# Optimization experiments

Measured on AMD Instinct MI355X. Metric: run time of the kernel, lower is better.

The kernel has to match this reference:

```python
import jax, jax.numpy as jnp
import numpy as np

E = 23  # unique experts
K = 3   # activated experts per token


def setup_inputs() -> dict:
    key = jax.random.key(0)
    ks = jax.random.split(key, 8)
    B, S, D, H = 4, 1024, 1024, 768
    sd = 1.0 / np.sqrt(D)
    sh = 1.0 / np.sqrt(H)
    return {
        "x": jax.random.normal(ks[0], (B, S, D), jnp.float32),
        "gate_W": jax.random.normal(ks[1], (D, E), jnp.float32) * sd,
        "gate_b": jnp.zeros((E,), jnp.float32),
        "route_bias": jnp.zeros((E,), jnp.float32),  # registered buffer 'bias'
        "W1": jax.random.normal(ks[2], (E, D, H), jnp.float32) * sd,
        "b1": jnp.zeros((E, H), jnp.float32),
        "W2": jax.random.normal(ks[3], (E, H, D), jnp.float32) * sh,
        "b2": jnp.zeros((E, D), jnp.float32),
        "sW1": jax.random.normal(ks[4], (D, H), jnp.float32) * sd,
        "sb1": jnp.zeros((H,), jnp.float32),
        "sW2": jax.random.normal(ks[5], (H, D), jnp.float32) * sh,
        "sb2": jnp.zeros((D,), jnp.float32),
    }


def _gelu(x):
    return jax.nn.gelu(x, approximate=False)  # torch nn.GELU default = exact erf


def reference(x, gate_W, gate_b, route_bias, W1, b1, W2, b2, sW1, sb1, sW2, sb2):
    o_shape = x.shape
    xt = x.reshape(-1, o_shape[-1])                       # [N, D]
    N = xt.shape[0]
    gate_weights = jax.nn.sigmoid(xt @ gate_W + gate_b)   # [N, E]
    _, top_idx = jax.lax.top_k(gate_weights + route_bias, K)  # [N, K]
    top_w = jnp.take_along_axis(gate_weights, top_idx, axis=-1)
    top_w = top_w / top_w.sum(axis=-1, keepdims=True)     # [N, K]
    onehot = jax.nn.one_hot(top_idx, E, dtype=xt.dtype)   # [N, K, E]
    combine = jnp.einsum('nke,nk->ne', onehot, top_w)     # [N, E] routed weights
    counts = onehot.sum(axis=(0, 1))                      # tokens per expert
    # dense-equivalent grouped expert MLPs (same math as gather/split/concat)
    h = _gelu(jnp.einsum('nd,edh->enh', xt, W1) + b1[:, None, :])   # [E, N, H]
    y = jnp.einsum('enh,ehd->end', h, W2) + b2[:, None, :]          # [E, N, D]
    routed = jnp.einsum('end,ne->nd', y, combine)
    shared = _gelu(xt @ sW1 + sb1) @ sW2 + sb2
    out = shared + routed
    # aux load-balance loss
    gw_norm = gate_weights / gate_weights.sum(axis=-1, keepdims=True)
    P = gw_norm.mean(axis=0)
    Fvec = (E * counts) / (K * N)
    aux_loss = (P * Fvec).sum()
    return out.reshape(o_shape), aux_loss
```

## Files before the change

kernel.cpp:

```cpp
#include <hip/hip_runtime.h>
#include <hip/hip_bf16.h>
#include <stdint.h>

#define N_TOK 4096
#define DDIM  1024
#define HDIM  768
#define NEXP  23
#define TOPK  3
#define MAXTILE 152
#define SLOTS   19456

typedef float floatx4 __attribute__((ext_vector_type(4)));
typedef short short8  __attribute__((ext_vector_type(8)));

__device__ __forceinline__ short f2bf(float f) {
    __hip_bfloat16 h = __float2bfloat16(f);
    return *reinterpret_cast<short*>(&h);
}
__device__ __forceinline__ float bf2f(short s) {
    unsigned u = ((unsigned)(unsigned short)s) << 16;
    return __uint_as_float(u);
}
__device__ __forceinline__ float gelu_erf(float v) {
    return 0.5f * v * (1.0f + erff(v * 0.70710678118654752f));
}
__device__ __forceinline__ void gl_lds16(const short* g, short* l) {
    __builtin_amdgcn_global_load_lds(
        (const __attribute__((address_space(1))) void*)g,
        (__attribute__((address_space(3))) void*)l, 16, 0, 0);
}

__global__ __launch_bounds__(256) void gate_kernel(
    const float* __restrict__ x, const float* __restrict__ gate_W,
    const float* __restrict__ gate_b, const float* __restrict__ route_bias,
    int* __restrict__ top_idx, float* __restrict__ top_w,
    float* __restrict__ psum_part)
{
    const int wave = threadIdx.x >> 6, lane = threadIdx.x & 63;
    const int n = blockIdx.x * 4 + wave;

    __shared__ float gw[64][25];
    float acc[NEXP];
#pragma unroll
    for (int e = 0; e < NEXP; e++) acc[e] = 0.f;

    const float* xr = x + (size_t)n * DDIM;
    for (int c0 = 0; c0 < DDIM; c0 += 64) {
        for (int idx = threadIdx.x; idx < 64 * NEXP; idx += 256)
            gw[idx / NEXP][idx % NEXP] = gate_W[(size_t)c0 * NEXP + idx];
        __syncthreads();
        float xd = xr[c0 + lane];
#pragma unroll
        for (int e = 0; e < NEXP; e++) acc[e] += xd * gw[lane][e];
        __syncthreads();
    }
    for (int off = 32; off > 0; off >>= 1) {
#pragma unroll
        for (int e = 0; e < NEXP; e++) acc[e] += __shfl_xor(acc[e], off, 64);
    }

    float p[NEXP], s = 0.f;
#pragma unroll
    for (int e = 0; e < NEXP; e++) {
        p[e] = 1.f / (1.f + expf(-(acc[e] + gate_b[e])));
        s += p[e];
    }
    const float inv = 1.f / s;

    __shared__ float ps[4][NEXP];
    if (lane == 0) {
#pragma unroll
        for (int e = 0; e < NEXP; e++) ps[wave][e] = p[e] * inv;
        int idx[TOPK]; float w[TOPK]; bool used[NEXP] = {};
        for (int k = 0; k < TOPK; k++) {
            float best = -1e30f; int bi = 0;
            for (int e = 0; e < NEXP; e++) {
                if (!used[e]) {
                    float sc = p[e] + route_bias[e];
                    if (sc > best) { best = sc; bi = e; }
                }
            }
            used[bi] = true; idx[k] = bi; w[k] = p[bi];
        }
        float wsum = w[0] + w[1] + w[2];
        for (int k = 0; k < TOPK; k++) {
            top_idx[n * TOPK + k] = idx[k];
            top_w[n * TOPK + k]   = w[k] / wsum;
        }
    }
    __syncthreads();
    if (threadIdx.x < NEXP) {
        int e = threadIdx.x;
        psum_part[(size_t)blockIdx.x * NEXP + e] =
            ps[0][e] + ps[1][e] + ps[2][e] + ps[3][e];
    }
}

__global__ __launch_bounds__(256) void plan_kernel(
    const int* __restrict__ top_idx, const float* __restrict__ psum_part,
    int* __restrict__ poff, int* __restrict__ cursor, int* __restrict__ tile_e,
    int* __restrict__ Ptot, float* __restrict__ out_aux)
{
    __shared__ int   cnt[NEXP];
    __shared__ float psum[NEXP];
    const int t = threadIdx.x;
    if (t < NEXP) { cnt[t] = 0; psum[t] = 0.f; }
    __syncthreads();

    for (int i = t; i < N_TOK * TOPK; i += 256)
        atomicAdd(&cnt[top_idx[i]], 1);

    float loc[NEXP];
#pragma unroll
    for (int e = 0; e < NEXP; e++) loc[e] = 0.f;
    for (int b = t; b < N_TOK / 4; b += 256) {
        const float* row = psum_part + (size_t)b * NEXP;
#pragma unroll
        for (int e = 0; e < NEXP; e++) loc[e] += row[e];
    }
#pragma unroll
    for (int e = 0; e < NEXP; e++) atomicAdd(&psum[e], loc[e]);
    __syncthreads();

    if (t == 0) {
        int off = 0, nt = 0; float aux = 0.f;
        for (int e = 0; e < NEXP; e++) {
            poff[e] = off; cursor[e] = 0;
            float P = psum[e] / (float)N_TOK;
            float F = (float)NEXP * (float)cnt[e] / ((float)TOPK * (float)N_TOK);
            aux += P * F;
            int tiles = (cnt[e] + 127) >> 7;
            for (int i = 0; i < tiles; i++) tile_e[nt++] = e;
            off += tiles << 7;
        }
        poff[NEXP] = off;
        *Ptot = off;
        for (int i = 0; i < N_TOK / 128; i++) tile_e[nt++] = NEXP;
        while (nt < MAXTILE) tile_e[nt++] = -1;
        *out_aux = aux;
    }
}

__global__ __launch_bounds__(256) void scatter_kernel(
    const int* __restrict__ top_idx, const int* __restrict__ poff,
    int* __restrict__ cursor, int* __restrict__ tok_of_slot,
    int* __restrict__ slot_of_tok)
{
    int n = blockIdx.x * 256 + threadIdx.x;
    for (int k = 0; k < TOPK; k++) {
        int e = top_idx[n * TOPK + k];
        int pos = atomicAdd(&cursor[e], 1);
        int slot = poff[e] + pos;
        tok_of_slot[slot] = n;
        slot_of_tok[n * 4 + k] = slot;
    }
}

__global__ __launch_bounds__(256) void fillshared_kernel(
    const int* __restrict__ Ptot, int* __restrict__ tok_of_slot,
    int* __restrict__ slot_of_tok)
{
    int n = blockIdx.x * 256 + threadIdx.x;
    int P = *Ptot;
    tok_of_slot[P + n] = n;
    slot_of_tok[n * 4 + 3] = P + n;
}

__global__ __launch_bounds__(256) void xcvt_kernel(
    const float* __restrict__ x, short* __restrict__ xb)
{
    size_t i = (size_t)blockIdx.x * 256 + threadIdx.x;
    float4 v = ((const float4*)x)[i];
    short4 o;
    o.x = f2bf(v.x); o.y = f2bf(v.y); o.z = f2bf(v.z); o.w = f2bf(v.w);
    ((short4*)xb)[i] = o;
    if (blockIdx.x == 0) {
        short4 z; z.x = 0; z.y = 0; z.z = 0; z.w = 0;
        ((short4*)(xb + (size_t)N_TOK * DDIM))[threadIdx.x] = z;
    }
}

__global__ __launch_bounds__(256) void tcvt_kernel(
    const float* __restrict__ src, short* __restrict__ dst, int R, int C)
{
    __shared__ short tile[64][66];
    const float* s = src + (size_t)blockIdx.z * R * C;
    short* d = dst + (size_t)blockIdx.z * R * C;
    const int c0 = blockIdx.x * 64, r0 = blockIdx.y * 64;
    const int tc = threadIdx.x & 63, tq = threadIdx.x >> 6;

    for (int i = 0; i < 64; i += 4) {
        int r = i + tq;
        tile[tc][r] = f2bf(s[(size_t)(r0 + r) * C + c0 + tc]);
    }
    __syncthreads();
    for (int j = 0; j < 64; j += 4) {
        int c = j + tq;
        d[(size_t)(c0 + c) * R + r0 + tc] = tile[c][tc];
    }
}

__global__ __launch_bounds__(256) void biascat_kernel(
    const float* __restrict__ b1, const float* __restrict__ sb1,
    const float* __restrict__ b2, const float* __restrict__ sb2,
    float* __restrict__ bias1_all, float* __restrict__ bias2_all)
{
    int i = blockIdx.x * 256 + threadIdx.x;
    if (i < 24 * HDIM) {
        bias1_all[i] = (i < NEXP * HDIM) ? b1[i] : sb1[i - NEXP * HDIM];
    } else {
        int j = i - 24 * HDIM;
        bias2_all[j] = (j < NEXP * DDIM) ? b2[j] : sb2[j - NEXP * DDIM];
    }
}

template <bool FFN1>
__global__ __launch_bounds__(256) void gemm_kernel(
    const short* __restrict__ Abase, const int* __restrict__ tok_of_slot,
    const int* __restrict__ tile_e, const short* __restrict__ Wall,
    const float* __restrict__ bias_all, const short* __restrict__ zrow,
    short* __restrict__ outb)
{
    constexpr int KD = FFN1 ? DDIM : HDIM;
    constexpr int NC = FFN1 ? HDIM : DDIM;

    const int tile = blockIdx.y;
    const int e = tile_e[tile];
    if (e < 0) return;
    const int slot0 = tile * 128;
    const int n0 = blockIdx.x * 128;

    __shared__ short As[128 * 32];
    __shared__ short Bs[128 * 32];

    const int t = threadIdx.x;
    const int w = t >> 6, l = t & 63;
    const int quad = l >> 4, l16 = l & 15;
    const int wr = w >> 1, wc = w & 1;

    const int ra0 = w * 32 + (l >> 2);
    const int ra1 = ra0 + 16;
    const int ko  = (l & 3) << 3;

    const short *ap0, *ap1;
    if constexpr (FFN1) {
        int t0 = tok_of_slot[slot0 + ra0];
        int t1 = tok_of_slot[slot0 + ra1];
        ap0 = (t0 >= 0) ? Abase + (size_t)t0 * KD : zrow;
        ap1 = (t1 >= 0) ? Abase + (size_t)t1 * KD : zrow;
    } else {
        ap0 = Abase + (size_t)(slot0 + ra0) * KD;
        ap1 = Abase + (size_t)(slot0 + ra1) * KD;
    }
    ap0 += ko; ap1 += ko;
    const short* bbase = Wall + (size_t)e * NC * KD + (size_t)n0 * KD;
    const short* bp0 = bbase + (size_t)ra0 * KD + ko;
    const short* bp1 = bbase + (size_t)ra1 * KD + ko;

    short* asd0 = As + (w * 32) * 32;
    short* asd1 = As + (w * 32 + 16) * 32;
    short* bsd0 = Bs + (w * 32) * 32;
    short* bsd1 = Bs + (w * 32 + 16) * 32;

    floatx4 acc[4][4] = {};

    for (int k0 = 0; k0 < KD; k0 += 32) {
        gl_lds16(ap0, asd0); gl_lds16(ap1, asd1);
        gl_lds16(bp0, bsd0); gl_lds16(bp1, bsd1);
        ap0 += 32; ap1 += 32; bp0 += 32; bp1 += 32;
        __syncthreads();

        short8 af[4], bf[4];
#pragma unroll
        for (int i = 0; i < 4; i++)
            af[i] = *(const short8*)&As[(wr * 64 + i * 16 + l16) * 32 + quad * 8];
#pragma unroll
        for (int j = 0; j < 4; j++)
            bf[j] = *(const short8*)&Bs[(wc * 64 + j * 16 + l16) * 32 + quad * 8];
#pragma unroll
        for (int i = 0; i < 4; i++)
#pragma unroll
            for (int j = 0; j < 4; j++)
                acc[i][j] = __builtin_amdgcn_mfma_f32_16x16x32_bf16(af[i], bf[j], acc[i][j], 0, 0, 0);
        __syncthreads();
    }

    const int bias_off = e * NC;
#pragma unroll
    for (int j = 0; j < 4; j++) {
        const int col = n0 + wc * 64 + j * 16 + l16;
        const float bv = bias_all[bias_off + col];
#pragma unroll
        for (int i = 0; i < 4; i++)
#pragma unroll
            for (int r = 0; r < 4; r++) {
                const int row = slot0 + wr * 64 + i * 16 + quad * 4 + r;
                float v = acc[i][j][r] + bv;
                outb[(size_t)row * NC + col] = f2bf(FFN1 ? gelu_erf(v) : v);
            }
    }
}

__global__ __launch_bounds__(256) void combine_kernel(
    const short* __restrict__ ybuf, const int* __restrict__ slot_of_tok,
    const float* __restrict__ top_w, float* __restrict__ out)
{
    const int n = blockIdx.x;
    const int c = threadIdx.x;
    const int s0 = slot_of_tok[n * 4 + 0];
    const int s1 = slot_of_tok[n * 4 + 1];
    const int s2 = slot_of_tok[n * 4 + 2];
    const int ss = slot_of_tok[n * 4 + 3];
    const float w0 = top_w[n * 3 + 0];
    const float w1 = top_w[n * 3 + 1];
    const float w2 = top_w[n * 3 + 2];

    short4 y0 = ((const short4*)(ybuf + (size_t)s0 * DDIM))[c];
    short4 y1 = ((const short4*)(ybuf + (size_t)s1 * DDIM))[c];
    short4 y2 = ((const short4*)(ybuf + (size_t)s2 * DDIM))[c];
    short4 ys = ((const short4*)(ybuf + (size_t)ss * DDIM))[c];

    float4 o;
    o.x = bf2f(ys.x) + w0 * bf2f(y0.x) + w1 * bf2f(y1.x) + w2 * bf2f(y2.x);
    o.y = bf2f(ys.y) + w0 * bf2f(y0.y) + w1 * bf2f(y1.y) + w2 * bf2f(y2.y);
    o.z = bf2f(ys.z) + w0 * bf2f(y0.z) + w1 * bf2f(y1.z) + w2 * bf2f(y2.z);
    o.w = bf2f(ys.w) + w0 * bf2f(y0.w) + w1 * bf2f(y1.w) + w2 * bf2f(y2.w);
    ((float4*)(out + (size_t)n * DDIM))[c] = o;
}

extern "C" void kernel_launch(void* const* d_in, const int* in_sizes, int n_in,
                              void* d_out, int out_size, void* d_ws, size_t ws_size,
                              hipStream_t stream)
{
    const float* x          = (const float*)d_in[0];
    const float* gate_W     = (const float*)d_in[1];
    const float* gate_b     = (const float*)d_in[2];
    const float* route_bias = (const float*)d_in[3];
    const float* W1         = (const float*)d_in[4];
    const float* b1         = (const float*)d_in[5];
    const float* W2         = (const float*)d_in[6];
    const float* b2         = (const float*)d_in[7];
    const float* sW1        = (const float*)d_in[8];
    const float* sb1        = (const float*)d_in[9];
    const float* sW2        = (const float*)d_in[10];
    const float* sb2        = (const float*)d_in[11];
    float* out = (float*)d_out;

    uint8_t* ws = (uint8_t*)d_ws;
    int*   top_idx   = (int*)(ws);
    float* top_w     = (float*)(ws + 49152);
    int*   poff      = (int*)(ws + 98304);
    int*   cursor    = (int*)(ws + 98432);
    int*   Ptot      = (int*)(ws + 98560);
    int*   tile_e    = (int*)(ws + 98688);
    float* psum_part = (float*)(ws + 99328);
    int*   tok_slot  = (int*)(ws + 193536);
    int*   slot_tok  = (int*)(ws + 271360);
    float* bias1_all = (float*)(ws + 336896);
    float* bias2_all = (float*)(ws + 410624);
    short* xb        = (short*)(ws + 512000);
    short* W1T       = (short*)(ws + 8902656);
    short* W2T       = (short*)(ws + 46651392);
    short* hbuf      = (short*)(ws + 84400128);
    short* ybuf      = (short*)(ws + 512000);
    const short* zrow = xb + (size_t)N_TOK * DDIM;

    hipMemsetAsync(tok_slot, 0xFF, SLOTS * sizeof(int), stream);

    xcvt_kernel<<<N_TOK * DDIM / 4 / 256, 256, 0, stream>>>(x, xb);
    tcvt_kernel<<<dim3(HDIM / 64, DDIM / 64, NEXP), 256, 0, stream>>>(W1, W1T, DDIM, HDIM);
    tcvt_kernel<<<dim3(HDIM / 64, DDIM / 64, 1), 256, 0, stream>>>(
        sW1, W1T + (size_t)NEXP * DDIM * HDIM, DDIM, HDIM);
    tcvt_kernel<<<dim3(DDIM / 64, HDIM / 64, NEXP), 256, 0, stream>>>(W2, W2T, HDIM, DDIM);
    tcvt_kernel<<<dim3(DDIM / 64, HDIM / 64, 1), 256, 0, stream>>>(
        sW2, W2T + (size_t)NEXP * HDIM * DDIM, HDIM, DDIM);
    biascat_kernel<<<(24 * HDIM + 24 * DDIM) / 256, 256, 0, stream>>>(
        b1, sb1, b2, sb2, bias1_all, bias2_all);

    gate_kernel<<<N_TOK / 4, 256, 0, stream>>>(x, gate_W, gate_b, route_bias,
                                               top_idx, top_w, psum_part);
    plan_kernel<<<1, 256, 0, stream>>>(top_idx, psum_part, poff, cursor, tile_e,
                                       Ptot, out + (size_t)N_TOK * DDIM);
    scatter_kernel<<<N_TOK / 256, 256, 0, stream>>>(top_idx, poff, cursor,
                                                    tok_slot, slot_tok);
    fillshared_kernel<<<N_TOK / 256, 256, 0, stream>>>(Ptot, tok_slot, slot_tok);

    gemm_kernel<true><<<dim3(HDIM / 128, MAXTILE), 256, 0, stream>>>(
        xb, tok_slot, tile_e, W1T, bias1_all, zrow, hbuf);
    gemm_kernel<false><<<dim3(DDIM / 128, MAXTILE), 256, 0, stream>>>(
        hbuf, tok_slot, tile_e, W2T, bias2_all, zrow, ybuf);
    combine_kernel<<<N_TOK, 256, 0, stream>>>(ybuf, slot_tok, top_w, out);
}
```

Measured before the change: 503.1 us.

## Vectorize weight transpose-convert and merge small prep launches

New measurement: 492.6 us. 1.02x faster.

```diff
diff --git a/kernel.cpp b/kernel.cpp
--- a/kernel.cpp
+++ b/kernel.cpp
@@ -144,7 +144,7 @@
 __global__ __launch_bounds__(256) void scatter_kernel(
     const int* __restrict__ top_idx, const int* __restrict__ poff,
     int* __restrict__ cursor, int* __restrict__ tok_of_slot,
-    int* __restrict__ slot_of_tok)
+    int* __restrict__ slot_of_tok, const int* __restrict__ Ptot)
 {
     int n = blockIdx.x * 256 + threadIdx.x;
     for (int k = 0; k < TOPK; k++) {
@@ -154,63 +154,65 @@
         tok_of_slot[slot] = n;
         slot_of_tok[n * 4 + k] = slot;
     }
-}
-
-__global__ __launch_bounds__(256) void fillshared_kernel(
-    const int* __restrict__ Ptot, int* __restrict__ tok_of_slot,
-    int* __restrict__ slot_of_tok)
-{
-    int n = blockIdx.x * 256 + threadIdx.x;
     int P = *Ptot;
     tok_of_slot[P + n] = n;
     slot_of_tok[n * 4 + 3] = P + n;
 }
 
-__global__ __launch_bounds__(256) void xcvt_kernel(
-    const float* __restrict__ x, short* __restrict__ xb)
-{
-    size_t i = (size_t)blockIdx.x * 256 + threadIdx.x;
-    float4 v = ((const float4*)x)[i];
-    short4 o;
-    o.x = f2bf(v.x); o.y = f2bf(v.y); o.z = f2bf(v.z); o.w = f2bf(v.w);
-    ((short4*)xb)[i] = o;
-    if (blockIdx.x == 0) {
-        short4 z; z.x = 0; z.y = 0; z.z = 0; z.w = 0;
-        ((short4*)(xb + (size_t)N_TOK * DDIM))[threadIdx.x] = z;
-    }
-}
-
-__global__ __launch_bounds__(256) void tcvt_kernel(
-    const float* __restrict__ src, short* __restrict__ dst, int R, int C)
-{
-    __shared__ short tile[64][66];
-    const float* s = src + (size_t)blockIdx.z * R * C;
-    short* d = dst + (size_t)blockIdx.z * R * C;
-    const int c0 = blockIdx.x * 64, r0 = blockIdx.y * 64;
-    const int tc = threadIdx.x & 63, tq = threadIdx.x >> 6;
-
-    for (int i = 0; i < 64; i += 4) {
-        int r = i + tq;
-        tile[tc][r] = f2bf(s[(size_t)(r0 + r) * C + c0 + tc]);
-    }
-    __syncthreads();
-    for (int j = 0; j < 64; j += 4) {
-        int c = j + tq;
-        d[(size_t)(c0 + c) * R + r0 + tc] = tile[c][tc];
-    }
-}
-
-__global__ __launch_bounds__(256) void biascat_kernel(
+__global__ __launch_bounds__(256) void prep_kernel(
+    const float* __restrict__ x, short* __restrict__ xb,
     const float* __restrict__ b1, const float* __restrict__ sb1,
     const float* __restrict__ b2, const float* __restrict__ sb2,
     float* __restrict__ bias1_all, float* __restrict__ bias2_all)
 {
-    int i = blockIdx.x * 256 + threadIdx.x;
-    if (i < 24 * HDIM) {
-        bias1_all[i] = (i < NEXP * HDIM) ? b1[i] : sb1[i - NEXP * HDIM];
+    const int b = blockIdx.x;
+    if (b < N_TOK) {
+        size_t i = (size_t)b * 256 + threadIdx.x;
+        float4 v = ((const float4*)x)[i];
+        short4 o;
+        o.x = f2bf(v.x); o.y = f2bf(v.y); o.z = f2bf(v.z); o.w = f2bf(v.w);
+        ((short4*)xb)[i] = o;
+    } else if (b == N_TOK) {
+        short4 z; z.x = 0; z.y = 0; z.z = 0; z.w = 0;
+        ((short4*)(xb + (size_t)N_TOK * DDIM))[threadIdx.x] = z;
     } else {
-        int j = i - 24 * HDIM;
-        bias2_all[j] = (j < NEXP * DDIM) ? b2[j] : sb2[j - NEXP * DDIM];
+        int i = (b - N_TOK - 1) * 256 + threadIdx.x;
+        if (i < 24 * HDIM) {
+            bias1_all[i] = (i < NEXP * HDIM) ? b1[i] : sb1[i - NEXP * HDIM];
+        } else {
+            int j = i - 24 * HDIM;
+            if (j < 24 * DDIM)
+                bias2_all[j] = (j < NEXP * DDIM) ? b2[j] : sb2[j - NEXP * DDIM];
+        }
+    }
+}
+
+__global__ __launch_bounds__(256) void tcvt_kernel(
+    const float* __restrict__ src, const float* __restrict__ ssrc,
+    short* __restrict__ dst, int R, int C)
+{
+    __shared__ short tile[64][72];
+    const int e = blockIdx.z;
+    const float* s = (e < NEXP) ? src + (size_t)e * R * C : ssrc;
+    short* d = dst + (size_t)e * R * C;
+    const int c0 = blockIdx.x * 64, r0 = blockIdx.y * 64;
+    const int t = threadIdx.x;
+
+    const int rr = t >> 4, cc = (t & 15) << 2;
+#pragma unroll
+    for (int i = 0; i < 64; i += 16) {
+        float4 v = *(const float4*)&s[(size_t)(r0 + i + rr) * C + c0 + cc];
+        tile[cc + 0][i + rr] = f2bf(v.x);
+        tile[cc + 1][i + rr] = f2bf(v.y);
+        tile[cc + 2][i + rr] = f2bf(v.z);
+        tile[cc + 3][i + rr] = f2bf(v.w);
+    }
+    __syncthreads();
+    const int cc2 = t >> 3, rr2 = (t & 7) << 3;
+#pragma unroll
+    for (int j = 0; j < 64; j += 32) {
+        *(short8*)&d[(size_t)(c0 + j + cc2) * R + r0 + rr2] =
+            *(const short8*)&tile[j + cc2][rr2];
     }
 }
 
@@ -367,23 +369,19 @@
 
     hipMemsetAsync(tok_slot, 0xFF, SLOTS * sizeof(int), stream);
 
-    xcvt_kernel<<<N_TOK * DDIM / 4 / 256, 256, 0, stream>>>(x, xb);
-    tcvt_kernel<<<dim3(HDIM / 64, DDIM / 64, NEXP), 256, 0, stream>>>(W1, W1T, DDIM, HDIM);
-    tcvt_kernel<<<dim3(HDIM / 64, DDIM / 64, 1), 256, 0, stream>>>(
-        sW1, W1T + (size_t)NEXP * DDIM * HDIM, DDIM, HDIM);
-    tcvt_kernel<<<dim3(DDIM / 64, HDIM / 64, NEXP), 256, 0, stream>>>(W2, W2T, HDIM, DDIM);
-    tcvt_kernel<<<dim3(DDIM / 64, HDIM / 64, 1), 256, 0, stream>>>(
-        sW2, W2T + (size_t)NEXP * HDIM * DDIM, HDIM, DDIM);
-    biascat_kernel<<<(24 * HDIM + 24 * DDIM) / 256, 256, 0, stream>>>(
-        b1, sb1, b2, sb2, bias1_all, bias2_all);
+    prep_kernel<<<N_TOK + 1 + (24 * (HDIM + DDIM) + 255) / 256, 256, 0, stream>>>(
+        x, xb, b1, sb1, b2, sb2, bias1_all, bias2_all);
+    tcvt_kernel<<<dim3(HDIM / 64, DDIM / 64, 24), 256, 0, stream>>>(
+        W1, sW1, W1T, DDIM, HDIM);
+    tcvt_kernel<<<dim3(DDIM / 64, HDIM / 64, 24), 256, 0, stream>>>(
+        W2, sW2, W2T, HDIM, DDIM);
 
     gate_kernel<<<N_TOK / 4, 256, 0, stream>>>(x, gate_W, gate_b, route_bias,
                                                top_idx, top_w, psum_part);
     plan_kernel<<<1, 256, 0, stream>>>(top_idx, psum_part, poff, cursor, tile_e,
                                        Ptot, out + (size_t)N_TOK * DDIM);
     scatter_kernel<<<N_TOK / 256, 256, 0, stream>>>(top_idx, poff, cursor,
-                                                    tok_slot, slot_tok);
-    fillshared_kernel<<<N_TOK / 256, 256, 0, stream>>>(Ptot, tok_slot, slot_tok);
+                                                    tok_slot, slot_tok, Ptot);
 
     gemm_kernel<true><<<dim3(HDIM / 128, MAXTILE), 256, 0, stream>>>(
         xb, tok_slot, tile_e, W1T, bias1_all, zrow, hbuf);
```
